# Performance work log

Measured on AMD Instinct MI355X. Metric: run time of the kernel, lower is better.

The kernel has to match this reference:

```python
import jax, jax.numpy as jnp
import numpy as np

K = 6
N_LEVELS = [200000, 50000, 12500]
CHANNELS = [3, 64, 128, 256]
DEGREE = 32
FANIN = 4          # each pooled node averages FANIN fine nodes (D values = 1/FANIN)
NUM_CLASSES = 10


def setup_inputs() -> dict:
    key = jax.random.key(0)
    ks = jax.random.split(key, 16)
    inp = {}
    inp["x"] = jax.random.normal(ks[0], (N_LEVELS[0], 3), dtype=jnp.float32)
    # random sparse connectivity per level (edge lists, COO)
    for i, n in enumerate(N_LEVELS):
        inp[f"edge_index{i}"] = jax.random.randint(ks[1 + i], (2, n * DEGREE), 0, n)
    # sparse downscale matrices: row r of D_i averages FANIN source nodes
    inp["pool_cols0"] = jax.random.randint(ks[4], (N_LEVELS[1] * FANIN,), 0, N_LEVELS[0])
    inp["pool_cols1"] = jax.random.randint(ks[5], (N_LEVELS[2] * FANIN,), 0, N_LEVELS[1])
    # ChebConv parameters: weight [K, in, out] (Glorot-ish), bias [out]
    for i in range(3):
        cin, cout = CHANNELS[i], CHANNELS[i + 1]
        scale = (2.0 / (cin + cout)) ** 0.5
        inp[f"w{i}"] = scale * jax.random.normal(ks[6 + 2 * i], (K, cin, cout), dtype=jnp.float32)
        inp[f"b{i}"] = jnp.zeros((cout,), dtype=jnp.float32)
    lin_in = N_LEVELS[-1] * CHANNELS[-1]
    inp["lw"] = jax.random.normal(ks[12], (NUM_CLASSES, lin_in), dtype=jnp.float32) * (1.0 / np.sqrt(lin_in))
    inp["lb"] = jnp.zeros((NUM_CLASSES,), dtype=jnp.float32)
    return inp


def cheb_conv(x, edge_index, weight, bias):
    """PyG ChebConv, sym normalization, lambda_max=2, unit edge weights.
    Scaled Laplacian reduces to L_hat = -D^{-1/2} A D^{-1/2} (zero diagonal)."""
    row, col = edge_index[0], edge_index[1]
    n = x.shape[0]
    w = (row != col).astype(x.dtype)                 # remove_self_loops
    deg = jax.ops.segment_sum(w, row, num_segments=n)
    dinv = jnp.where(deg > 0, jax.lax.rsqrt(deg), 0.0)
    norm = -w * dinv[row] * dinv[col]                # [E]

    def prop(h):  # scatter-add of norm * gathered source features
        return jax.ops.segment_sum(norm[:, None] * h[col], row, num_segments=n)

    Tx0 = x
    out = Tx0 @ weight[0]
    Tx1 = prop(x)
    out = out + Tx1 @ weight[1]
    for k in range(2, weight.shape[0]):
        Tx2 = 2.0 * prop(Tx1) - Tx0
        out = out + Tx2 @ weight[k]
        Tx0, Tx1 = Tx1, Tx2
    return out + bias


def pool(x, cols, n_out):
    # sparse.mm(D, x) with D having FANIN entries of 1/FANIN per row (rows sorted)
    return x[cols].reshape(n_out, FANIN, x.shape[1]).mean(axis=1)


def reference(x, edge_index0, edge_index1, edge_index2, pool_cols0, pool_cols1,
              w0, b0, w1, b1, w2, b2, lw, lb):
    h = jax.nn.relu(cheb_conv(x, edge_index0, w0, b0))
    h = pool(h, pool_cols0, N_LEVELS[1])
    h = jax.nn.relu(cheb_conv(h, edge_index1, w1, b1))
    h = pool(h, pool_cols1, N_LEVELS[2])
    h = cheb_conv(h, edge_index2, w2, b2)
    return lw @ h.reshape(-1) + lb   # F.linear on flattened features -> [num_classes]
```

## Files before the change

kernel.cpp:

```cpp
#include <hip/hip_runtime.h>
#include <hip/hip_bf16.h>


#define N0 200000
#define N1 50000
#define N2 12500
#define KCH 6
#define NCLS 10

#define SB 8
#define BROWS 256
#define BCAP 10240
#define NBUK_MAX 800
#define NBLK 1024
#define TILE_MAX 6250

typedef __hip_bfloat16 bf16;
typedef _Float16 f16;
typedef f16 f16x2 __attribute__((ext_vector_type(2)));
typedef f16 f16x4 __attribute__((ext_vector_type(4)));
typedef f16 f16x8 __attribute__((ext_vector_type(8)));
typedef float f32x4 __attribute__((ext_vector_type(4)));

static __device__ __forceinline__ float b2f(bf16 v) { return __bfloat162float(v); }
static __device__ __forceinline__ float blo(unsigned u) { return __uint_as_float(u << 16); }
static __device__ __forceinline__ float bhi(unsigned u) { return __uint_as_float(u & 0xFFFF0000u); }

struct BLvl {
    const int* rows; const int* cols;
    int* cntBB; int* cntScan; int* btot; int* bbase;
    unsigned* colB; int* colS; int* ptr; float* dinv;
    int E, nbuk, tile, n;
};

__global__ void detect_k(const unsigned int* __restrict__ xb, int* __restrict__ flag) {
    __shared__ int cs;
    int t = threadIdx.x;
    if (t == 0) cs = 0;
    __syncthreads();
    unsigned w = xb[t];
    unsigned e = (w >> 7) & 0xFFu;
    if (e >= 0x30u && e <= 0x43u) atomicAdd(&cs, 1);
    __syncthreads();
    if (t == 0) flag[0] = (cs < 128) ? 1 : 0;
}

__global__ __launch_bounds__(256) void convw2_k(const void* __restrict__ W1, f16* __restrict__ wT1,
                                                const void* __restrict__ W2, f16* __restrict__ wT2,
                                                const int* __restrict__ flag) {
    int isf = flag[0];
    int idx = blockIdx.x * 256 + threadIdx.x;
    const int tot1 = 384 * 128;
    const int tot2 = 768 * 256;
    if (idx < tot1) {
        int n2 = idx / 384, k = idx - n2 * 384;
        float v;
        if (isf) v = ((const float*)W1)[(size_t)k * 128 + n2];
        else     v = b2f(((const bf16*)W1)[(size_t)k * 128 + n2]);
        wT1[idx] = (f16)v;
    } else if (idx < tot1 + tot2) {
        int i2 = idx - tot1;
        int n2 = i2 / 768, k = i2 - n2 * 768;
        float v;
        if (isf) v = ((const float*)W2)[(size_t)k * 256 + n2];
        else     v = b2f(((const bf16*)W2)[(size_t)k * 256 + n2]);
        wT2[i2] = (f16)v;
    }
}


__global__ __launch_bounds__(256) void binH3_k(BLvl a, BLvl b, BLvl c) {
    BLvl lv = (blockIdx.y == 0) ? a : ((blockIdx.y == 1) ? b : c);
    __shared__ int cnt[NBUK_MAX];
    int t = threadIdx.x;
    for (int i = t; i < lv.nbuk; i += 256) cnt[i] = 0;
    __syncthreads();
    int beg = blockIdx.x * lv.tile;
    int end = beg + lv.tile;
    if (end > lv.E) end = lv.E;
    for (int idx = beg + t; idx < end; idx += 256) {
        int r = lv.rows[idx], cc = lv.cols[idx];
        if (r != cc) atomicAdd(&cnt[r >> SB], 1);
    }
    __syncthreads();
    for (int i = t; i < lv.nbuk; i += 256) lv.cntBB[(size_t)blockIdx.x * lv.nbuk + i] = cnt[i];
}

__global__ __launch_bounds__(256) void scanBB3_k(BLvl a, BLvl b, BLvl c) {
    __shared__ int ps[256];
    int gb = blockIdx.x, t = threadIdx.x;
    BLvl lv; int b0;
    if (gb < a.nbuk) { lv = a; b0 = gb; }
    else if (gb < a.nbuk + b.nbuk) { lv = b; b0 = gb - a.nbuk; }
    else { lv = c; b0 = gb - a.nbuk - b.nbuk; }
    int vals[4];
    int pt = 0;
#pragma unroll
    for (int i = 0; i < 4; ++i) { vals[i] = lv.cntBB[(size_t)(4 * t + i) * lv.nbuk + b0]; pt += vals[i]; }
    ps[t] = pt;
    __syncthreads();
    for (int off = 1; off < 256; off <<= 1) {
        int x = (t >= off) ? ps[t - off] : 0;
        __syncthreads();
        ps[t] += x;
        __syncthreads();
    }
    int ex = ps[t] - pt;
#pragma unroll
    for (int i = 0; i < 4; ++i) { lv.cntScan[(size_t)(4 * t + i) * lv.nbuk + b0] = ex; ex += vals[i]; }
    if (t == 255) lv.btot[b0] = ps[255];
}

__global__ __launch_bounds__(1024) void scanb3_k(BLvl a, BLvl b, BLvl c, float* __restrict__ accum) {
    __shared__ int s[1024];
    BLvl lv = (blockIdx.x == 0) ? a : ((blockIdx.x == 1) ? b : c);
    int t = threadIdx.x;
    if (blockIdx.x == 0 && t < 16) accum[t] = 0.f;
    int v = (t < lv.nbuk) ? lv.btot[t] : 0;
    s[t] = v;
    __syncthreads();
    for (int off = 1; off < 1024; off <<= 1) {
        int x = (t >= off) ? s[t - off] : 0;
        __syncthreads();
        s[t] += x;
        __syncthreads();
    }
    if (t < lv.nbuk) lv.bbase[t] = s[t] - v;
    if (t == 1023) lv.ptr[lv.n] = s[1023];
}

__global__ __launch_bounds__(256) void binS3_k(BLvl a, BLvl b, BLvl c) {
    BLvl lv = (blockIdx.y == 0) ? a : ((blockIdx.y == 1) ? b : c);
    __shared__ int lcnt[NBUK_MAX];
    __shared__ int lexc[NBUK_MAX];
    __shared__ int lfill[NBUK_MAX];
    __shared__ int gstart[NBUK_MAX];
    __shared__ int ps[256];
    __shared__ unsigned scol[TILE_MAX];
    int t = threadIdx.x;
    for (int i = t; i < lv.nbuk; i += 256) {
        lcnt[i] = lv.cntBB[(size_t)blockIdx.x * lv.nbuk + i];
        lfill[i] = 0;
        gstart[i] = lv.bbase[i] + lv.cntScan[(size_t)blockIdx.x * lv.nbuk + i];
    }
    __syncthreads();
    int beg = blockIdx.x * lv.tile;
    int end = beg + lv.tile;
    if (end > lv.E) end = lv.E;
    int idx4 = 4 * t;
    int c4[4];
#pragma unroll
    for (int i = 0; i < 4; ++i) c4[i] = (idx4 + i < lv.nbuk) ? lcnt[idx4 + i] : 0;
    int tot = c4[0] + c4[1] + c4[2] + c4[3];
    ps[t] = tot;
    __syncthreads();
    for (int off = 1; off < 256; off <<= 1) {
        int x = (t >= off) ? ps[t - off] : 0;
        __syncthreads();
        ps[t] += x;
        __syncthreads();
    }
    int run = ps[t] - tot;
#pragma unroll
    for (int i = 0; i < 4; ++i) {
        if (idx4 + i < lv.nbuk) lexc[idx4 + i] = run;
        run += c4[i];
    }
    __syncthreads();
    for (int idx = beg + t; idx < end; idx += 256) {
        int r = lv.rows[idx], cc = lv.cols[idx];
        if (r != cc) {
            int bk = r >> SB;
            int s = atomicAdd(&lfill[bk], 1);
            scol[lexc[bk] + s] = ((unsigned)(r & (BROWS - 1)) << 18) | (unsigned)cc;
        }
    }
    __syncthreads();
    int grp = t >> 3, gl = t & 7;
    for (int bk = grp; bk < lv.nbuk; bk += 32) {
        int cnt2 = lcnt[bk];
        int lsrc = lexc[bk], gdst = gstart[bk];
        for (int i = gl; i < cnt2; i += 8) lv.colB[gdst + i] = scol[lsrc + i];
    }
}

__global__ __launch_bounds__(256) void binB3_k(BLvl a, BLvl b, BLvl c,
                                               const void* __restrict__ x, f16* __restrict__ TxAll,
                                               f16x4* __restrict__ G0, const int* __restrict__ flag) {
    __shared__ int lcnt[BROWS];
    __shared__ int lexc[BROWS];
    __shared__ int lfill[BROWS];
    __shared__ int scol[BCAP];
    int gb = blockIdx.x;
    int t = threadIdx.x;
    BLvl lv; int b0, lvl;
    if (gb < a.nbuk) { lv = a; b0 = gb; lvl = 0; }
    else if (gb < a.nbuk + b.nbuk) { lv = b; b0 = gb - a.nbuk; lvl = 1; }
    else { lv = c; b0 = gb - a.nbuk - b.nbuk; lvl = 2; }
    int rowbase = b0 << SB;
    int rowend = rowbase + BROWS;
    if (rowend > lv.n) rowend = lv.n;
    int nrows = rowend - rowbase;
    int count = lv.btot[b0];
    int base = lv.bbase[b0];
    const unsigned* slab = lv.colB + base;
    lcnt[t] = 0;
    __syncthreads();
    for (int i = t; i < count; i += 256) atomicAdd(&lcnt[slab[i] >> 18], 1);
    __syncthreads();
    int v = lcnt[t];
    lexc[t] = v;
    __syncthreads();
    for (int off = 1; off < 256; off <<= 1) {
        int xx = (t >= off) ? lexc[t - off] : 0;
        __syncthreads();
        lexc[t] += xx;
        __syncthreads();
    }
    int excl = lexc[t] - v;
    __syncthreads();
    lexc[t] = excl;
    __syncthreads();
    if (t < nrows) {
        lv.ptr[rowbase + t] = base + excl;
        float dr = (v > 0) ? rsqrtf((float)v) : 0.f;
        lv.dinv[rowbase + t] = dr;
        if (lvl == 0) {
            int r = rowbase + t;
            int isf = flag[0];
            float v0, v1, v2;
            if (isf) {
                const float* xf = (const float*)x;
                v0 = xf[3 * r]; v1 = xf[3 * r + 1]; v2 = xf[3 * r + 2];
            } else {
                const bf16* xh = (const bf16*)x;
                v0 = b2f(xh[3 * r]); v1 = b2f(xh[3 * r + 1]); v2 = b2f(xh[3 * r + 2]);
            }
            f16x4 pk = {(f16)v0, (f16)v1, (f16)v2, (f16)dr};
            *(f16x4*)(TxAll + (size_t)r * 24) = pk;
            G0[r] = pk;
        }
    }
    int nh = (count <= BCAP) ? 1 : 2;
    int rspan = BROWS / nh;
    for (int h = 0; h < nh; ++h) {
        int rowLo = h * rspan, rowHi = rowLo + rspan;
        int segOff = lexc[rowLo];
        int segEnd = (rowHi >= BROWS) ? count : lexc[rowHi];
        int segCnt = segEnd - segOff;
        lfill[t] = 0;
        __syncthreads();
        for (int i = t; i < count; i += 256) {
            unsigned pk = slab[i];
            int rl = pk >> 18;
            if (rl >= rowLo && rl < rowHi) {
                int s = atomicAdd(&lfill[rl], 1);
                scol[lexc[rl] + s - segOff] = (int)(pk & 0x3FFFFu);
            }
        }
        __syncthreads();
        for (int i = t; i < segCnt; i += 256) lv.colS[base + segOff + i] = scol[i];
        __syncthreads();
    }
}


__global__ __launch_bounds__(256) void prop_narrow_k(const int* __restrict__ ptr, const int* __restrict__ colS,
                                                     const float* __restrict__ dinv,
                                                     const f16x4* __restrict__ gin, f16x4* __restrict__ gout,
                                                     f16* __restrict__ oslot,
                                                     int n, float alpha, int useSub) {
    int wv = threadIdx.x >> 6, half = (threadIdx.x >> 5) & 1, sl = threadIdx.x & 31;
    int r = blockIdx.x * 8 + wv * 2 + half;
    if (r >= n) return;
    int s = ptr[r], e = ptr[r + 1];
    float dr = dinv[r];
    float a0 = 0.f, a1 = 0.f, a2 = 0.f;
    for (int idx = s + sl; idx < e; idx += 32) {
        int c = colS[idx];
        f16x4 h = gin[c];
        float nrm = -dr * (float)h.w;
        a0 += nrm * (float)h.x;
        a1 += nrm * (float)h.y;
        a2 += nrm * (float)h.z;
    }
#pragma unroll
    for (int off2 = 16; off2 > 0; off2 >>= 1) {
        a0 += __shfl_xor(a0, off2);
        a1 += __shfl_xor(a1, off2);
        a2 += __shfl_xor(a2, off2);
    }
    if (sl == 0) {
        float v0 = alpha * a0, v1 = alpha * a1, v2 = alpha * a2;
        if (useSub) {
            f16x4 sv = gout[r];
            v0 -= (float)sv.x; v1 -= (float)sv.y; v2 -= (float)sv.z;
        }
        f16x4 ov = {(f16)v0, (f16)v1, (f16)v2, (f16)dr};
        gout[r] = ov;
        *(f16x4*)(oslot + (size_t)r * 24) = ov;
    }
}

__global__ __launch_bounds__(256) void prop_wide2_k(const int* __restrict__ ptr, const int* __restrict__ colS,
                                                    const float* __restrict__ dinv, const f16* __restrict__ hin,
                                                    const f16* __restrict__ sub, f16* __restrict__ o,
                                                    int ld, int n, float alpha, int useSub) {
    int wv = threadIdx.x >> 6, lane = threadIdx.x & 63;
    int p = lane >> 5, q = lane & 31;
    int r = blockIdx.x * 4 + wv;
    if (r >= n) return;
    int s = ptr[r], e = ptr[r + 1];
    float dr = dinv[r];
    float ax = 0.f, ay = 0.f;
    for (int base = s; base < e; base += 64) {
        int idx = base + lane;
        int c = 0;
        float dc = 0.f;
        if (idx < e) { c = colS[idx]; dc = dinv[c]; }
        int cnt2 = e - base;
        if (cnt2 > 64) cnt2 = 64;
        int j = 0;
        for (; j + 4 <= cnt2; j += 4) {
            int j0 = j + p, j1 = j + 2 + p;
            int c0 = __shfl(c, j0), c1 = __shfl(c, j1);
            float n0 = -dr * __shfl(dc, j0), n1 = -dr * __shfl(dc, j1);
            f16x2 h0 = *(const f16x2*)(hin + (size_t)c0 * ld + 2 * q);
            f16x2 h1 = *(const f16x2*)(hin + (size_t)c1 * ld + 2 * q);
            ax += n0 * (float)h0.x + n1 * (float)h1.x;
            ay += n0 * (float)h0.y + n1 * (float)h1.y;
        }
        for (; j < cnt2; j += 2) {
            int jj = j + p;
            int valid = jj < cnt2;
            int cc = __shfl(c, valid ? jj : 0);
            float nd = __shfl(dc, valid ? jj : 0);
            float nrm = valid ? -dr * nd : 0.f;
            f16x2 h = *(const f16x2*)(hin + (size_t)cc * ld + 2 * q);
            ax += nrm * (float)h.x;
            ay += nrm * (float)h.y;
        }
    }
    ax += __shfl_xor(ax, 32);
    ay += __shfl_xor(ay, 32);
    if (p == 0) {
        size_t rb = (size_t)r * ld + 2 * q;
        float vx = alpha * ax, vy = alpha * ay;
        if (useSub) {
            f16x2 sv = *(const f16x2*)(sub + rb);
            vx -= (float)sv.x; vy -= (float)sv.y;
        }
        f16x2 ov = {(f16)vx, (f16)vy};
        *(f16x2*)(o + rb) = ov;
    }
}

__global__ __launch_bounds__(256) void prop_wide1h_k(const int* __restrict__ ptr, const int* __restrict__ colS,
                                                     const float* __restrict__ dinv, const f16* __restrict__ hin,
                                                     const f16* __restrict__ sub, f16* __restrict__ o,
                                                     int ld, int n, float alpha, int useSub) {
    int wv = threadIdx.x >> 6, lane = threadIdx.x & 63;
    int r = blockIdx.x * 4 + wv;
    if (r >= n) return;
    int s = ptr[r], e = ptr[r + 1];
    float dr = dinv[r];
    float ax = 0.f, ay = 0.f;
    for (int base = s; base < e; base += 64) {
        int idx = base + lane;
        int c = 0;
        float dc = 0.f;
        if (idx < e) { c = colS[idx]; dc = dinv[c]; }
        int cnt2 = e - base;
        if (cnt2 > 64) cnt2 = 64;
        int j = 0;
        for (; j + 4 <= cnt2; j += 4) {
            int c0 = __shfl(c, j), c1 = __shfl(c, j + 1), c2 = __shfl(c, j + 2), c3 = __shfl(c, j + 3);
            float n0 = -dr * __shfl(dc, j), n1 = -dr * __shfl(dc, j + 1);
            float n2 = -dr * __shfl(dc, j + 2), n3 = -dr * __shfl(dc, j + 3);
            f16x2 h0 = *(const f16x2*)(hin + (size_t)c0 * ld + 2 * lane);
            f16x2 h1 = *(const f16x2*)(hin + (size_t)c1 * ld + 2 * lane);
            f16x2 h2 = *(const f16x2*)(hin + (size_t)c2 * ld + 2 * lane);
            f16x2 h3 = *(const f16x2*)(hin + (size_t)c3 * ld + 2 * lane);
            ax += n0 * (float)h0.x + n1 * (float)h1.x + n2 * (float)h2.x + n3 * (float)h3.x;
            ay += n0 * (float)h0.y + n1 * (float)h1.y + n2 * (float)h2.y + n3 * (float)h3.y;
        }
        for (; j < cnt2; ++j) {
            int cc = __shfl(c, j);
            float nrm = -dr * __shfl(dc, j);
            f16x2 h = *(const f16x2*)(hin + (size_t)cc * ld + 2 * lane);
            ax += nrm * (float)h.x;
            ay += nrm * (float)h.y;
        }
    }
    size_t rb = (size_t)r * ld + 2 * lane;
    float vx = alpha * ax, vy = alpha * ay;
    if (useSub) {
        f16x2 sv = *(const f16x2*)(sub + rb);
        vx -= (float)sv.x; vy -= (float)sv.y;
    }
    f16x2 ov = {(f16)vx, (f16)vy};
    *(f16x2*)(o + rb) = ov;
}


__global__ __launch_bounds__(256) void gemm_mfma2_k(const f16* __restrict__ A, int lda,
                                                    const f16* __restrict__ WT,
                                                    const void* __restrict__ bias,
                                                    void* __restrict__ C, int M, int N, int K, int flags,
                                                    const int* __restrict__ flag) {
    __shared__ f16 As[64][40];
    __shared__ f16 Bs[64][40];
    int isf = flag[0];
    int t = threadIdx.x;
    int w = t >> 6, l = t & 63, q = l >> 4, m16 = l & 15;
    int m0 = blockIdx.y * 64, n0 = blockIdx.x * 64;
    f32x4 acc[4] = {};
    for (int k0 = 0; k0 < K; k0 += 32) {
        {
            int row = t >> 2, cg = (t & 3) * 8;
            int gm = m0 + row;
            f16x8 av = {};
            if (gm < M) av = *(const f16x8*)(A + (size_t)gm * lda + k0 + cg);
            *(f16x8*)&As[row][cg] = av;
        }
        {
            int nr = t >> 2, cg = (t & 3) * 8;
            f16x8 bv = *(const f16x8*)(WT + (size_t)(n0 + nr) * K + k0 + cg);
            *(f16x8*)&Bs[nr][cg] = bv;
        }
        __syncthreads();
        f16x8 aa = *(const f16x8*)&As[w * 16 + m16][q * 8];
        f16x8 b0 = *(const f16x8*)&Bs[m16][q * 8];
        f16x8 b1 = *(const f16x8*)&Bs[16 + m16][q * 8];
        f16x8 b2 = *(const f16x8*)&Bs[32 + m16][q * 8];
        f16x8 b3 = *(const f16x8*)&Bs[48 + m16][q * 8];
        acc[0] = __builtin_amdgcn_mfma_f32_16x16x32_f16(aa, b0, acc[0], 0, 0, 0);
        acc[1] = __builtin_amdgcn_mfma_f32_16x16x32_f16(aa, b1, acc[1], 0, 0, 0);
        acc[2] = __builtin_amdgcn_mfma_f32_16x16x32_f16(aa, b2, acc[2], 0, 0, 0);
        acc[3] = __builtin_amdgcn_mfma_f32_16x16x32_f16(aa, b3, acc[3], 0, 0, 0);
        __syncthreads();
    }
#pragma unroll
    for (int tile = 0; tile < 4; ++tile) {
        int gn = n0 + tile * 16 + m16;
        float bv = 0.f;
        if (flags & 4) {
            if (isf) bv = ((const float*)bias)[gn];
            else     bv = b2f(((const bf16*)bias)[gn]);
        }
#pragma unroll
        for (int i = 0; i < 4; ++i) {
            int gm = m0 + w * 16 + q * 4 + i;
            if (gm < M) {
                float v = acc[tile][i] + bv;
                if (flags & 1) v = fmaxf(v, 0.f);
                size_t ci = (size_t)gm * N + gn;
                if (flags & 16) ((f16*)C)[ci] = (f16)v;
                else            ((float*)C)[ci] = v;
            }
        }
    }
}


__global__ __launch_bounds__(256) void gemm_k(const f16* __restrict__ A, int lda,
                                              const void* __restrict__ W,
                                              const void* __restrict__ bias,
                                              void* __restrict__ C, int M, int N, int K, int flags,
                                              const int* __restrict__ flag) {
    __shared__ float As[16][65];
    __shared__ float Ws[16][64];
    int isf = flag[0];
    int pack3 = flags & 8;
    int t = threadIdx.x;
    int tn = t & 15, tm = t >> 4;
    int m0 = blockIdx.y * 64, n0 = blockIdx.x * 64;
    float acc[4][4] = {};
    for (int k0 = 0; k0 < K; k0 += 16) {
#pragma unroll
        for (int i = 0; i < 4; ++i) {
            int idx = i * 256 + t;
            int m = idx >> 4, k = idx & 15;
            int gm = m0 + m, gk = k0 + k;
            int phys = pack3 ? (gk + gk / 3) : gk;
            As[k][m] = (gm < M && gk < K) ? (float)A[(size_t)gm * lda + phys] : 0.f;
        }
        if (isf) {
            const float* Wf = (const float*)W;
#pragma unroll
            for (int i = 0; i < 4; ++i) {
                int idx = i * 256 + t;
                int k = idx >> 6, nn = idx & 63;
                int gk = k0 + k;
                Ws[k][nn] = (gk < K) ? Wf[(size_t)gk * N + n0 + nn] : 0.f;
            }
        } else {
            const bf16* Wh = (const bf16*)W;
#pragma unroll
            for (int i = 0; i < 4; ++i) {
                int idx = i * 256 + t;
                int k = idx >> 6, nn = idx & 63;
                int gk = k0 + k;
                Ws[k][nn] = (gk < K) ? b2f(Wh[(size_t)gk * N + n0 + nn]) : 0.f;
            }
        }
        __syncthreads();
#pragma unroll
        for (int kk = 0; kk < 16; ++kk) {
            float aa[4], bb[4];
#pragma unroll
            for (int i = 0; i < 4; ++i) aa[i] = As[kk][tm * 4 + i];
#pragma unroll
            for (int j = 0; j < 4; ++j) bb[j] = Ws[kk][tn * 4 + j];
#pragma unroll
            for (int i = 0; i < 4; ++i)
#pragma unroll
                for (int j = 0; j < 4; ++j) acc[i][j] += aa[i] * bb[j];
        }
        __syncthreads();
    }
#pragma unroll
    for (int i = 0; i < 4; ++i) {
        int gm = m0 + tm * 4 + i;
        if (gm >= M) continue;
#pragma unroll
        for (int j = 0; j < 4; ++j) {
            int gn = n0 + tn * 4 + j;
            size_t ci = (size_t)gm * N + gn;
            float v = acc[i][j];
            if (flags & 4) {
                if (isf) v += ((const float*)bias)[gn];
                else     v += b2f(((const bf16*)bias)[gn]);
            }
            if (flags & 1) v = fmaxf(v, 0.f);
            if (flags & 16) ((f16*)C)[ci] = (f16)v;
            else            ((float*)C)[ci] = v;
        }
    }
}


__global__ __launch_bounds__(256) void pool_k(const f16* __restrict__ in, const int* __restrict__ pcols,
                                              f16* __restrict__ out, int n_out, int C, int ld) {
    int idx = blockIdx.x * 256 + threadIdx.x;
    int C4 = C >> 2;
    if (idx >= n_out * C4) return;
    int r = idx / C4, c4 = (idx - r * C4) * 4;
    const int* pc = pcols + (size_t)r * 4;
    float s0 = 0.f, s1 = 0.f, s2 = 0.f, s3 = 0.f;
#pragma unroll
    for (int f = 0; f < 4; ++f) {
        f16x4 v = *(const f16x4*)(in + (size_t)pc[f] * C + c4);
        s0 += (float)v.x; s1 += (float)v.y; s2 += (float)v.z; s3 += (float)v.w;
    }
    f16x4 o = {(f16)(0.25f * s0), (f16)(0.25f * s1), (f16)(0.25f * s2), (f16)(0.25f * s3)};
    *(f16x4*)(out + (size_t)r * ld + c4) = o;
}


__global__ __launch_bounds__(256) void linear10b_k(const float* __restrict__ h, const void* __restrict__ lw,
                                                   float* __restrict__ accum, int LIN, const int* __restrict__ flag) {
    int isf = flag[0];
    int t = threadIdx.x;
    int nvec = LIN >> 3;
    int stride = gridDim.x * 256;
    float p[NCLS];
#pragma unroll
    for (int c = 0; c < NCLS; ++c) p[c] = 0.f;
    const float4* h4 = (const float4*)h;
    if (isf) {
        const float4* lw4 = (const float4*)lw;
        size_t ro = (size_t)(LIN >> 2);
        for (int i = blockIdx.x * 256 + t; i < nvec; i += stride) {
            float4 a0 = h4[2 * i], a1 = h4[2 * i + 1];
#pragma unroll
            for (int c = 0; c < NCLS; ++c) {
                float4 b0v = lw4[c * ro + 2 * i], b1v = lw4[c * ro + 2 * i + 1];
                p[c] += a0.x * b0v.x + a0.y * b0v.y + a0.z * b0v.z + a0.w * b0v.w
                      + a1.x * b1v.x + a1.y * b1v.y + a1.z * b1v.z + a1.w * b1v.w;
            }
        }
    } else {
        const uint4* lwv = (const uint4*)lw;
        size_t ro = (size_t)nvec;
        for (int i = blockIdx.x * 256 + t; i < nvec; i += stride) {
            float4 a0 = h4[2 * i], a1 = h4[2 * i + 1];
#pragma unroll
            for (int c = 0; c < NCLS; ++c) {
                uint4 w4 = lwv[c * ro + i];
                p[c] += a0.x * blo(w4.x) + a0.y * bhi(w4.x)
                      + a0.z * blo(w4.y) + a0.w * bhi(w4.y)
                      + a1.x * blo(w4.z) + a1.y * bhi(w4.z)
                      + a1.z * blo(w4.w) + a1.w * bhi(w4.w);
            }
        }
    }
    __shared__ float wsum[4][NCLS];
    int wv = t >> 6, lane = t & 63;
#pragma unroll
    for (int c = 0; c < NCLS; ++c) {
        float v = p[c];
        for (int off2 = 32; off2 > 0; off2 >>= 1) v += __shfl_down(v, off2);
        if (lane == 0) wsum[wv][c] = v;
    }
    __syncthreads();
    if (t < NCLS) {
        float s = wsum[0][t] + wsum[1][t] + wsum[2][t] + wsum[3][t];
        unsafeAtomicAdd(&accum[t], s);
    }
}

__global__ void finalize_k(const float* __restrict__ accum, const void* __restrict__ lb,
                           void* __restrict__ outp, const int* __restrict__ flag) {
    int isf = flag[0];
    int t = threadIdx.x;
    if (t < NCLS) {
        float lbv;
        if (isf) lbv = ((const float*)lb)[t];
        else     lbv = b2f(((const bf16*)lb)[t]);
        float v = accum[t] + lbv;
        if (isf) ((float*)outp)[t] = v;
        else     ((bf16*)outp)[t] = __float2bfloat16(v);
    }
}

__global__ void diag_k(void* __restrict__ outp, float val, const int* __restrict__ flag) {
    int isf = flag[0];
    int t = threadIdx.x;
    if (t < NCLS) {
        if (isf) ((float*)outp)[t] = val;
        else     ((bf16*)outp)[t] = __float2bfloat16(val);
    }
}


extern "C" void kernel_launch(void* const* d_in, const int* in_sizes, int n_in,
                              void* d_out, int out_size, void* d_ws, size_t ws_size,
                              hipStream_t stream) {
    const void* x  = d_in[0];
    const int* ei0 = (const int*)d_in[1];
    const int* ei1 = (const int*)d_in[2];
    const int* ei2 = (const int*)d_in[3];
    const int* pc0 = (const int*)d_in[4];
    const int* pc1 = (const int*)d_in[5];
    const void* w0 = d_in[6];
    const void* b0 = d_in[7];
    const void* w1 = d_in[8];
    const void* b1 = d_in[9];
    const void* w2 = d_in[10];
    const void* b2 = d_in[11];
    const void* lw = d_in[12];
    const void* lb = d_in[13];

    const int E0 = in_sizes[1] / 2, E1 = in_sizes[2] / 2, E2 = in_sizes[3] / 2;
    const int Ns[3] = {N0, N1, N2};
    const int Es[3] = {E0, E1, E2};

    char* base = (char*)d_ws;
    size_t off = 0;
    auto alloc = [&](size_t bytes) -> void* {
        void* p = base + off;
        off += (bytes + 255) & ~(size_t)255;
        return p;
    };
    f16*      TxAll = (f16*)alloc((size_t)19200000 * 2);
    float*    OutB  = (float*)alloc((size_t)12800000 * 4);
    f16*      OutBh = (f16*)OutB;
    f16x4*    G0    = (f16x4*)alloc((size_t)N0 * 8);
    f16x4*    G1    = (f16x4*)alloc((size_t)N0 * 8);
    f16*      wT1   = (f16*)alloc((size_t)384 * 128 * 2);
    f16*      wT2   = (f16*)alloc((size_t)768 * 256 * 2);
    float*    accum = (float*)alloc(64);
    int*      flag  = (int*)(accum + 16);

    BLvl BL[3];
    for (int i = 0; i < 3; ++i) {
        int n = Ns[i], E = Es[i];
        BL[i].nbuk = (n + BROWS - 1) >> SB;
        BL[i].tile = (E + NBLK - 1) / NBLK;
        BL[i].E = E;
        BL[i].n = n;
        BL[i].cntBB   = (int*)alloc((size_t)NBLK * BL[i].nbuk * 4);
        BL[i].cntScan = (int*)alloc((size_t)NBLK * BL[i].nbuk * 4);
        BL[i].btot  = (int*)alloc((size_t)BL[i].nbuk * 4);
        BL[i].bbase = (int*)alloc((size_t)BL[i].nbuk * 4);
        BL[i].colB  = (unsigned*)alloc((size_t)E * 4);
        BL[i].colS  = (int*)alloc((size_t)E * 4);
        BL[i].ptr   = (int*)alloc((size_t)(n + 1) * 4);
        BL[i].dinv  = (float*)alloc((size_t)n * 4);
    }
    BL[0].rows = ei0; BL[0].cols = ei0 + E0;
    BL[1].rows = ei1; BL[1].cols = ei1 + E1;
    BL[2].rows = ei2; BL[2].cols = ei2 + E2;

    detect_k<<<1, 256, 0, stream>>>((const unsigned int*)x, flag);

    if (ws_size < off) {
        diag_k<<<1, 64, 0, stream>>>(d_out, (float)(ws_size >> 20), flag);
        return;
    }

    convw2_k<<<(384 * 128 + 768 * 256 + 255) / 256, 256, 0, stream>>>(w1, wT1, w2, wT2, flag);

    int nbukT = BL[0].nbuk + BL[1].nbuk + BL[2].nbuk;
    binH3_k<<<dim3(NBLK, 3), 256, 0, stream>>>(BL[0], BL[1], BL[2]);
    scanBB3_k<<<nbukT, 256, 0, stream>>>(BL[0], BL[1], BL[2]);
    scanb3_k<<<3, 1024, 0, stream>>>(BL[0], BL[1], BL[2], accum);
    binS3_k<<<dim3(NBLK, 3), 256, 0, stream>>>(BL[0], BL[1], BL[2]);
    binB3_k<<<nbukT, 256, 0, stream>>>(BL[0], BL[1], BL[2], x, TxAll, G0, flag);

    struct Lvl {
        int n, cin, cout;
        const void *w, *b;
        int relu;
    };
    Lvl L[3] = {
        {N0, 3, 64, w0, b0, 1},
        {N1, 64, 128, w1, b1, 1},
        {N2, 128, 256, w2, b2, 0},
    };
    f16x4* G[2] = {G0, G1};

    for (int li = 0; li < 3; ++li) {
        const Lvl& v = L[li];
        int n = v.n, cin = v.cin, cout = v.cout;
        int ld = (li == 0) ? 24 : KCH * cin;
        int slot = (li == 0) ? 4 : cin;
        const int* ptr = BL[li].ptr;
        const int* colS = BL[li].colS;
        const float* dinv = BL[li].dinv;

        for (int k = 1; k < KCH; ++k) {
            float alpha = (k >= 2) ? 2.f : 1.f;
            if (li == 0) {
                prop_narrow_k<<<(n + 7) / 8, 256, 0, stream>>>(ptr, colS, dinv,
                                                               G[(k - 1) & 1], G[k & 1],
                                                               TxAll + (size_t)k * 4, n, alpha, k >= 2);
            } else {
                const f16* hin = TxAll + (size_t)(k - 1) * slot;
                const f16* sub = (k >= 2) ? (TxAll + (size_t)(k - 2) * slot) : nullptr;
                f16* o = TxAll + (size_t)k * slot;
                if (cin == 64)
                    prop_wide2_k<<<(n + 3) / 4, 256, 0, stream>>>(ptr, colS, dinv, hin, sub, o, ld, n, alpha, k >= 2);
                else
                    prop_wide1h_k<<<(n + 3) / 4, 256, 0, stream>>>(ptr, colS, dinv, hin, sub, o, ld, n, alpha, k >= 2);
            }
        }

        dim3 gg(cout / 64, (n + 63) / 64);
        int f16out = (li < 2) ? 16 : 0;
        if (li == 0)
            gemm_k<<<gg, 256, 0, stream>>>(TxAll, ld, v.w, v.b, OutB, n, cout, KCH * cin,
                                           4 | 8 | f16out | (v.relu ? 1 : 0), flag);
        else
            gemm_mfma2_k<<<gg, 256, 0, stream>>>(TxAll, ld, (li == 1) ? wT1 : wT2, v.b, OutB, n, cout, KCH * cin,
                                                 4 | f16out | (v.relu ? 1 : 0), flag);

        if (li == 0)
            pool_k<<<(N1 * 16 + 255) / 256, 256, 0, stream>>>(OutBh, pc0, TxAll, N1, 64, KCH * 64);
        else if (li == 1)
            pool_k<<<(N2 * 32 + 255) / 256, 256, 0, stream>>>(OutBh, pc1, TxAll, N2, 128, KCH * 128);
    }

    {
        dim3 lg(512);
        linear10b_k<<<lg, 256, 0, stream>>>(OutB, lw, accum, N2 * 256, flag);
    }
    finalize_k<<<1, 64, 0, stream>>>(accum, lb, d_out, flag);
}
```

Before: 934.2 us.

## Fuse per-level Chebyshev propagation steps into one cooperative kernel with grid sync

Replaces the five separate propagation launches per level with a single cooperative kernel of 1024 blocks. The blocks loop over rows in grid-stride fashion and use grid.sync between Chebyshev orders. This removes four kernel launches and their gaps per level, 12 in total. In exchange, each level runs with a fixed persistent grid that may be less efficient than the full launch, and grid-wide barriers add their own cost. If the cooperative launch fails, the code falls back to the old per-step kernels.

```diff
diff --git a/kernel.cpp b/kernel.cpp
--- a/kernel.cpp
+++ b/kernel.cpp
@@ -1,5 +1,8 @@
 #include <hip/hip_runtime.h>
 #include <hip/hip_bf16.h>
+#include <hip/hip_cooperative_groups.h>
+
+namespace cg = cooperative_groups;
 
 
 #define N0 200000
@@ -14,6 +17,7 @@
 #define NBUK_MAX 800
 #define NBLK 1024
 #define TILE_MAX 6250
+#define COOPB 1024
 
 typedef __hip_bfloat16 bf16;
 typedef _Float16 f16;
@@ -261,6 +265,180 @@
         __syncthreads();
         for (int i = t; i < segCnt; i += 256) lv.colS[base + segOff + i] = scol[i];
         __syncthreads();
+    }
+}
+
+
+__global__ __launch_bounds__(256) void prop0f_k(const int* __restrict__ ptr, const int* __restrict__ colS,
+                                                const float* __restrict__ dinv,
+                                                f16x4* __restrict__ G0, f16x4* __restrict__ G1,
+                                                f16* __restrict__ Tx, int n) {
+    cg::grid_group grid = cg::this_grid();
+    int wv = threadIdx.x >> 6, half = (threadIdx.x >> 5) & 1, sl = threadIdx.x & 31;
+    int nvb = (n + 7) >> 3;
+    for (int k = 1; k < KCH; ++k) {
+        const f16x4* gin = (k & 1) ? G0 : G1;
+        f16x4* gout = (k & 1) ? G1 : G0;
+        f16* oslot = Tx + (size_t)k * 4;
+        float alpha = (k >= 2) ? 2.f : 1.f;
+        int useSub = (k >= 2);
+        for (int vb = blockIdx.x; vb < nvb; vb += gridDim.x) {
+            int r = vb * 8 + wv * 2 + half;
+            if (r < n) {
+                int s = ptr[r], e = ptr[r + 1];
+                float dr = dinv[r];
+                float a0 = 0.f, a1 = 0.f, a2 = 0.f;
+                for (int idx = s + sl; idx < e; idx += 32) {
+                    int c = colS[idx];
+                    f16x4 h = gin[c];
+                    float nrm = -dr * (float)h.w;
+                    a0 += nrm * (float)h.x;
+                    a1 += nrm * (float)h.y;
+                    a2 += nrm * (float)h.z;
+                }
+#pragma unroll
+                for (int off2 = 16; off2 > 0; off2 >>= 1) {
+                    a0 += __shfl_xor(a0, off2);
+                    a1 += __shfl_xor(a1, off2);
+                    a2 += __shfl_xor(a2, off2);
+                }
+                if (sl == 0) {
+                    float v0 = alpha * a0, v1 = alpha * a1, v2 = alpha * a2;
+                    if (useSub) {
+                        f16x4 sv = gout[r];
+                        v0 -= (float)sv.x; v1 -= (float)sv.y; v2 -= (float)sv.z;
+                    }
+                    f16x4 ov = {(f16)v0, (f16)v1, (f16)v2, (f16)dr};
+                    gout[r] = ov;
+                    *(f16x4*)(oslot + (size_t)r * 24) = ov;
+                }
+            }
+        }
+        if (k < KCH - 1) grid.sync();
+    }
+}
+
+__global__ __launch_bounds__(256) void prop1f_k(const int* __restrict__ ptr, const int* __restrict__ colS,
+                                                const float* __restrict__ dinv, f16* __restrict__ Tx,
+                                                int ld, int slot, int n) {
+    cg::grid_group grid = cg::this_grid();
+    int wv = threadIdx.x >> 6, lane = threadIdx.x & 63;
+    int p = lane >> 5, q = lane & 31;
+    int nvb = (n + 3) >> 2;
+    for (int k = 1; k < KCH; ++k) {
+        const f16* hin = Tx + (size_t)(k - 1) * slot;
+        const f16* sub = (k >= 2) ? (Tx + (size_t)(k - 2) * slot) : nullptr;
+        f16* o = Tx + (size_t)k * slot;
+        float alpha = (k >= 2) ? 2.f : 1.f;
+        int useSub = (k >= 2);
+        for (int vb = blockIdx.x; vb < nvb; vb += gridDim.x) {
+            int r = vb * 4 + wv;
+            if (r < n) {
+                int s = ptr[r], e = ptr[r + 1];
+                float dr = dinv[r];
+                float ax = 0.f, ay = 0.f;
+                for (int base = s; base < e; base += 64) {
+                    int idx = base + lane;
+                    int c = 0;
+                    float dc = 0.f;
+                    if (idx < e) { c = colS[idx]; dc = dinv[c]; }
+                    int cnt2 = e - base;
+                    if (cnt2 > 64) cnt2 = 64;
+                    int j = 0;
+                    for (; j + 4 <= cnt2; j += 4) {
+                        int j0 = j + p, j1 = j + 2 + p;
+                        int c0 = __shfl(c, j0), c1 = __shfl(c, j1);
+                        float n0 = -dr * __shfl(dc, j0), n1 = -dr * __shfl(dc, j1);
+                        f16x2 h0 = *(const f16x2*)(hin + (size_t)c0 * ld + 2 * q);
+                        f16x2 h1 = *(const f16x2*)(hin + (size_t)c1 * ld + 2 * q);
+                        ax += n0 * (float)h0.x + n1 * (float)h1.x;
+                        ay += n0 * (float)h0.y + n1 * (float)h1.y;
+                    }
+                    for (; j < cnt2; j += 2) {
+                        int jj = j + p;
+                        int valid = jj < cnt2;
+                        int cc = __shfl(c, valid ? jj : 0);
+                        float nd = __shfl(dc, valid ? jj : 0);
+                        float nrm = valid ? -dr * nd : 0.f;
+                        f16x2 h = *(const f16x2*)(hin + (size_t)cc * ld + 2 * q);
+                        ax += nrm * (float)h.x;
+                        ay += nrm * (float)h.y;
+                    }
+                }
+                ax += __shfl_xor(ax, 32);
+                ay += __shfl_xor(ay, 32);
+                if (p == 0) {
+                    size_t rb = (size_t)r * ld + 2 * q;
+                    float vx = alpha * ax, vy = alpha * ay;
+                    if (useSub) {
+                        f16x2 sv = *(const f16x2*)(sub + rb);
+                        vx -= (float)sv.x; vy -= (float)sv.y;
+                    }
+                    f16x2 ov = {(f16)vx, (f16)vy};
+                    *(f16x2*)(o + rb) = ov;
+                }
+            }
+        }
+        if (k < KCH - 1) grid.sync();
+    }
+}
+
+__global__ __launch_bounds__(256) void prop2f_k(const int* __restrict__ ptr, const int* __restrict__ colS,
+                                                const float* __restrict__ dinv, f16* __restrict__ Tx,
+                                                int ld, int slot, int n) {
+    cg::grid_group grid = cg::this_grid();
+    int wv = threadIdx.x >> 6, lane = threadIdx.x & 63;
+    int nvb = (n + 3) >> 2;
+    for (int k = 1; k < KCH; ++k) {
+        const f16* hin = Tx + (size_t)(k - 1) * slot;
+        const f16* sub = (k >= 2) ? (Tx + (size_t)(k - 2) * slot) : nullptr;
+        f16* o = Tx + (size_t)k * slot;
+        float alpha = (k >= 2) ? 2.f : 1.f;
+        int useSub = (k >= 2);
+        for (int vb = blockIdx.x; vb < nvb; vb += gridDim.x) {
+            int r = vb * 4 + wv;
+            if (r < n) {
+                int s = ptr[r], e = ptr[r + 1];
+                float dr = dinv[r];
+                float ax = 0.f, ay = 0.f;
+                for (int base = s; base < e; base += 64) {
+                    int idx = base + lane;
+                    int c = 0;
+                    float dc = 0.f;
+                    if (idx < e) { c = colS[idx]; dc = dinv[c]; }
+                    int cnt2 = e - base;
+                    if (cnt2 > 64) cnt2 = 64;
+                    int j = 0;
+                    for (; j + 4 <= cnt2; j += 4) {
+                        int c0 = __shfl(c, j), c1 = __shfl(c, j + 1), c2 = __shfl(c, j + 2), c3 = __shfl(c, j + 3);
+                        float n0 = -dr * __shfl(dc, j), n1 = -dr * __shfl(dc, j + 1);
+                        float n2 = -dr * __shfl(dc, j + 2), n3 = -dr * __shfl(dc, j + 3);
+                        f16x2 h0 = *(const f16x2*)(hin + (size_t)c0 * ld + 2 * lane);
+                        f16x2 h1 = *(const f16x2*)(hin + (size_t)c1 * ld + 2 * lane);
+                        f16x2 h2 = *(const f16x2*)(hin + (size_t)c2 * ld + 2 * lane);
+                        f16x2 h3 = *(const f16x2*)(hin + (size_t)c3 * ld + 2 * lane);
+                        ax += n0 * (float)h0.x + n1 * (float)h1.x + n2 * (float)h2.x + n3 * (float)h3.x;
+                        ay += n0 * (float)h0.y + n1 * (float)h1.y + n2 * (float)h2.y + n3 * (float)h3.y;
+                    }
+                    for (; j < cnt2; ++j) {
+                        int cc = __shfl(c, j);
+                        float nrm = -dr * __shfl(dc, j);
+                        f16x2 h = *(const f16x2*)(hin + (size_t)cc * ld + 2 * lane);
+                        ax += nrm * (float)h.x;
+                        ay += nrm * (float)h.y;
+                    }
+                }
+                size_t rb = (size_t)r * ld + 2 * lane;
+                float vx = alpha * ax, vy = alpha * ay;
+                if (useSub) {
+                    f16x2 sv = *(const f16x2*)(sub + rb);
+                    vx -= (float)sv.x; vy -= (float)sv.y;
+                }
+                f16x2 ov = {(f16)vx, (f16)vy};
+                *(f16x2*)(o + rb) = ov;
+            }
+        }
+        if (k < KCH - 1) grid.sync();
     }
 }
 
@@ -417,16 +595,16 @@
     f32x4 acc[4] = {};
     for (int k0 = 0; k0 < K; k0 += 32) {
         {
-            int row = t >> 2, cg = (t & 3) * 8;
+            int row = t >> 2, cg2 = (t & 3) * 8;
             int gm = m0 + row;
             f16x8 av = {};
-            if (gm < M) av = *(const f16x8*)(A + (size_t)gm * lda + k0 + cg);
-            *(f16x8*)&As[row][cg] = av;
+            if (gm < M) av = *(const f16x8*)(A + (size_t)gm * lda + k0 + cg2);
+            *(f16x8*)&As[row][cg2] = av;
         }
         {
-            int nr = t >> 2, cg = (t & 3) * 8;
-            f16x8 bv = *(const f16x8*)(WT + (size_t)(n0 + nr) * K + k0 + cg);
-            *(f16x8*)&Bs[nr][cg] = bv;
+            int nr = t >> 2, cg2 = (t & 3) * 8;
+            f16x8 bv = *(const f16x8*)(WT + (size_t)(n0 + nr) * K + k0 + cg2);
+            *(f16x8*)&Bs[nr][cg2] = bv;
         }
         __syncthreads();
         f16x8 aa = *(const f16x8*)&As[w * 16 + m16][q * 8];
@@ -730,20 +908,37 @@
         const int* colS = BL[li].colS;
         const float* dinv = BL[li].dinv;
 
-        for (int k = 1; k < KCH; ++k) {
-            float alpha = (k >= 2) ? 2.f : 1.f;
-            if (li == 0) {
-                prop_narrow_k<<<(n + 7) / 8, 256, 0, stream>>>(ptr, colS, dinv,
-                                                               G[(k - 1) & 1], G[k & 1],
-                                                               TxAll + (size_t)k * 4, n, alpha, k >= 2);
-            } else {
-                const f16* hin = TxAll + (size_t)(k - 1) * slot;
-                const f16* sub = (k >= 2) ? (TxAll + (size_t)(k - 2) * slot) : nullptr;
-                f16* o = TxAll + (size_t)k * slot;
-                if (cin == 64)
-                    prop_wide2_k<<<(n + 3) / 4, 256, 0, stream>>>(ptr, colS, dinv, hin, sub, o, ld, n, alpha, k >= 2);
-                else
-                    prop_wide1h_k<<<(n + 3) / 4, 256, 0, stream>>>(ptr, colS, dinv, hin, sub, o, ld, n, alpha, k >= 2);
+        bool coop = false;
+        if (li == 0) {
+            const int* ptrv = ptr; const int* colSv = colS; const float* dinvv = dinv;
+            f16x4* g0v = G0; f16x4* g1v = G1; f16* txv = TxAll; int nv = n;
+            void* args[] = {&ptrv, &colSv, &dinvv, &g0v, &g1v, &txv, &nv};
+            coop = (hipLaunchCooperativeKernel((const void*)prop0f_k, dim3(COOPB), dim3(256),
+                                               args, 0, stream) == hipSuccess);
+        } else {
+            const int* ptrv = ptr; const int* colSv = colS; const float* dinvv = dinv;
+            f16* txv = TxAll; int ldv = ld, slotv = slot, nv = n;
+            void* args[] = {&ptrv, &colSv, &dinvv, &txv, &ldv, &slotv, &nv};
+            const void* fn = (cin == 64) ? (const void*)prop1f_k : (const void*)prop2f_k;
+            coop = (hipLaunchCooperativeKernel(fn, dim3(COOPB), dim3(256),
+                                               args, 0, stream) == hipSuccess);
+        }
+        if (!coop) {
+            for (int k = 1; k < KCH; ++k) {
+                float alpha = (k >= 2) ? 2.f : 1.f;
+                if (li == 0) {
+                    prop_narrow_k<<<(n + 7) / 8, 256, 0, stream>>>(ptr, colS, dinv,
+                                                                   G[(k - 1) & 1], G[k & 1],
+                                                                   TxAll + (size_t)k * 4, n, alpha, k >= 2);
+                } else {
+                    const f16* hin = TxAll + (size_t)(k - 1) * slot;
+                    const f16* sub = (k >= 2) ? (TxAll + (size_t)(k - 2) * slot) : nullptr;
+                    f16* o = TxAll + (size_t)k * slot;
+                    if (cin == 64)
+                        prop_wide2_k<<<(n + 3) / 4, 256, 0, stream>>>(ptr, colS, dinv, hin, sub, o, ld, n, alpha, k >= 2);
+                    else
+                        prop_wide1h_k<<<(n + 3) / 4, 256, 0, stream>>>(ptr, colS, dinv, hin, sub, o, ld, n, alpha, k >= 2);
+                }
             }
         }
 
```

New measurement: 2.648 ms. 183% more time.
